# Optimization experiments

Hardware: AMD Instinct MI355X
Metric: run time of the kernel (lower is better)

## Reference

```python
import jax, jax.numpy as jnp
import numpy as np

M = 8192            # number of graphs (m)
NODES_PER_GRAPH = 64
N = M * NODES_PER_GRAPH  # total nodes (n)
D_H = 128
D_X = 128


def setup_inputs() -> dict:
    key = jax.random.key(0)
    k1, k2, k3 = jax.random.split(key, 3)
    # scale by 0.1 so the unstabilized exp(e) in segment_softmax stays finite in fp32
    h = 0.1 * jax.random.normal(k1, (M, D_H), dtype=jnp.float32)
    x = 0.1 * jax.random.normal(k2, (N, D_X), dtype=jnp.float32)
    a = jax.random.uniform(k3, (D_H, D_X), dtype=jnp.float32)  # th.rand init
    batch_num_nodes = jnp.full((M,), NODES_PER_GRAPH, dtype=jnp.int32)
    return {"h": h, "x": x, "a": a, "batch_num_nodes": batch_num_nodes}


def reference(h, x, a, batch_num_nodes):
    m = batch_num_nodes.shape[0]
    n = x.shape[0]
    # node -> graph segment ids (repeat_interleave of arange)
    seg = jnp.repeat(jnp.arange(m), batch_num_nodes, total_repeat_length=n)  # (n,)
    ha = (h @ a)[seg]                       # (n, d_x): gather per-graph query to nodes
    e = jnp.sum(x * ha, axis=1)             # (n,) attention logits
    ex = jnp.exp(e)                         # unstabilized exp, faithful to source
    z = jax.ops.segment_sum(ex, seg, num_segments=m)   # (m,) partition functions
    att = ex / z[seg]                       # (n,) segment softmax
    out = jax.ops.segment_sum(att[:, None] * x, seg, num_segments=m)  # (m, d_x)
    return out
```

## Files before the change

kernel.cpp:

```cpp
#include <hip/hip_runtime.h>


#define NPG  64
#define DDIM 128
#define SROW 132

typedef __attribute__((ext_vector_type(4))) float f32x4;

__global__ __launch_bounds__(256) void ha_gemm_kernel(
    const float* __restrict__ h, const float* __restrict__ a, float* __restrict__ ha)
{
    const int j    = threadIdx.x & 127;
    const int rg   = threadIdx.x >> 7;
    const int row0 = blockIdx.x * 8 + rg * 4;
    const float* hp = h + (size_t)row0 * DDIM;

    float acc0 = 0.f, acc1 = 0.f, acc2 = 0.f, acc3 = 0.f;
    #pragma unroll 8
    for (int k4 = 0; k4 < 32; ++k4) {
        f32x4 h0 = *(const f32x4*)(hp + 0 * DDIM + k4 * 4);
        f32x4 h1 = *(const f32x4*)(hp + 1 * DDIM + k4 * 4);
        f32x4 h2 = *(const f32x4*)(hp + 2 * DDIM + k4 * 4);
        f32x4 h3 = *(const f32x4*)(hp + 3 * DDIM + k4 * 4);
        #pragma unroll
        for (int kk = 0; kk < 4; ++kk) {
            float av = a[(k4 * 4 + kk) * DDIM + j];
            acc0 += h0[kk] * av;
            acc1 += h1[kk] * av;
            acc2 += h2[kk] * av;
            acc3 += h3[kk] * av;
        }
    }
    float* op = ha + (size_t)row0 * DDIM + j;
    op[0 * DDIM] = acc0; op[1 * DDIM] = acc1; op[2 * DDIM] = acc2; op[3 * DDIM] = acc3;
}

__global__ __launch_bounds__(256) void attn_kernel(
    const float* __restrict__ x, const float* __restrict__ ha, float* __restrict__ out)
{
    const int g = blockIdx.x;
    const int t = threadIdx.x;

    __shared__ __align__(16) float xs[NPG * SROW];
    __shared__ float exbuf[NPG];
    __shared__ float zbuf[4];
    __shared__ __align__(16) float opart[8][DDIM];

    const int qt = t & 3;
    const int i  = t >> 2;
    f32x4 qv[8];
    const float* qp = ha + (size_t)g * DDIM + qt * 32;
    #pragma unroll
    for (int c = 0; c < 8; ++c) qv[c] = *(const f32x4*)(qp + c * 4);

    const f32x4* xg = (const f32x4*)(x + (size_t)g * (NPG * DDIM));
    #pragma unroll
    for (int it = 0; it < 8; ++it) {
        int c = it * 256 + t;
        f32x4 v = xg[c];
        int row = c >> 5, col = c & 31;
        *(f32x4*)(&xs[row * SROW + col * 4]) = v;
    }
    __syncthreads();

    const float* xrow = &xs[i * SROW + qt * 32];
    float acc = 0.f;
    #pragma unroll
    for (int c = 0; c < 8; ++c) {
        f32x4 v = *(const f32x4*)(xrow + c * 4);
        acc += v[0] * qv[c][0] + v[1] * qv[c][1] + v[2] * qv[c][2] + v[3] * qv[c][3];
    }
    acc += __shfl_xor(acc, 1, 64);
    acc += __shfl_xor(acc, 2, 64);
    float ex = __expf(acc);
    float zw = ex;
    zw += __shfl_xor(zw, 4, 64);
    zw += __shfl_xor(zw, 8, 64);
    zw += __shfl_xor(zw, 16, 64);
    zw += __shfl_xor(zw, 32, 64);
    if (qt == 0)       exbuf[i] = ex;
    if ((t & 63) == 0) zbuf[t >> 6] = zw;
    __syncthreads();

    const float rz = 1.0f / (zbuf[0] + zbuf[1] + zbuf[2] + zbuf[3]);

    {
        const int jb  = (t & 31) * 4;
        const int grp = t >> 5;
        f32x4 o = {0.f, 0.f, 0.f, 0.f};
        #pragma unroll
        for (int k = 0; k < 8; ++k) {
            int node = grp * 8 + k;
            float w = exbuf[node] * rz;
            f32x4 v = *(const f32x4*)(&xs[node * SROW + jb]);
            o[0] += w * v[0]; o[1] += w * v[1]; o[2] += w * v[2]; o[3] += w * v[3];
        }
        *(f32x4*)(&opart[grp][jb]) = o;
    }
    __syncthreads();

    if (t < DDIM) {
        float o = 0.f;
        #pragma unroll
        for (int gq = 0; gq < 8; ++gq) o += opart[gq][t];
        out[(size_t)g * DDIM + t] = o;
    }
}

extern "C" void kernel_launch(void* const* d_in, const int* in_sizes, int n_in,
                              void* d_out, int out_size, void* d_ws, size_t ws_size,
                              hipStream_t stream) {
    const float* h = (const float*)d_in[0];
    const float* x = (const float*)d_in[1];
    const float* a = (const float*)d_in[2];
    float* out = (float*)d_out;
    float* ha  = (float*)d_ws;

    const int m = in_sizes[0] / DDIM;
    ha_gemm_kernel<<<m / 8, 256, 0, stream>>>(h, a, ha);
    attn_kernel<<<m, 256, 0, stream>>>(x, ha, out);
}
```

Before: 386.3 us.

## Keep node rows in registers and reduce weighted sum with wave shuffles

The attention kernel no longer stages the whole 64x128 graph tile in shared memory. Each thread loads its node's x slice directly into registers, computes the logit, and scales the slice by its softmax weight. The weighted sum is partially reduced across nodes with xor shuffles before a smaller shared-memory pass of 16 partials, and the launch bounds now request 6 blocks per CU. This cuts LDS traffic and footprint to raise occupancy, at the cost of many more shuffle instructions and higher register pressure.

```diff
diff --git a/kernel.cpp b/kernel.cpp
--- a/kernel.cpp
+++ b/kernel.cpp
@@ -3,7 +3,7 @@
 
 #define NPG  64
 #define DDIM 128
-#define SROW 132
+#define OROW 132
 
 typedef __attribute__((ext_vector_type(4))) float f32x4;
 
@@ -35,74 +35,71 @@
     op[0 * DDIM] = acc0; op[1 * DDIM] = acc1; op[2 * DDIM] = acc2; op[3 * DDIM] = acc3;
 }
 
-__global__ __launch_bounds__(256) void attn_kernel(
+__global__ __launch_bounds__(256, 6) void attn_kernel(
     const float* __restrict__ x, const float* __restrict__ ha, float* __restrict__ out)
 {
-    const int g = blockIdx.x;
-    const int t = threadIdx.x;
+    const int g  = blockIdx.x;
+    const int t  = threadIdx.x;
+    const int w  = t >> 6;
+    const int l  = t & 63;
+    const int i  = t >> 2;
+    const int qt = t & 3;
 
-    __shared__ __align__(16) float xs[NPG * SROW];
-    __shared__ float exbuf[NPG];
     __shared__ float zbuf[4];
-    __shared__ __align__(16) float opart[8][DDIM];
+    __shared__ __align__(16) float opart[16][OROW];
 
-    const int qt = t & 3;
-    const int i  = t >> 2;
-    f32x4 qv[8];
-    const float* qp = ha + (size_t)g * DDIM + qt * 32;
+    const float* xrow = x  + ((size_t)g * NPG + i) * DDIM;
+    const float* qrow = ha + (size_t)g * DDIM;
+    f32x4 xv[8];
     #pragma unroll
-    for (int c = 0; c < 8; ++c) qv[c] = *(const f32x4*)(qp + c * 4);
+    for (int c = 0; c < 8; ++c)
+        xv[c] = *(const f32x4*)(xrow + (qt + 4 * c) * 4);
 
-    const f32x4* xg = (const f32x4*)(x + (size_t)g * (NPG * DDIM));
-    #pragma unroll
-    for (int it = 0; it < 8; ++it) {
-        int c = it * 256 + t;
-        f32x4 v = xg[c];
-        int row = c >> 5, col = c & 31;
-        *(f32x4*)(&xs[row * SROW + col * 4]) = v;
-    }
-    __syncthreads();
-
-    const float* xrow = &xs[i * SROW + qt * 32];
-    float acc = 0.f;
+    float e = 0.f;
     #pragma unroll
     for (int c = 0; c < 8; ++c) {
-        f32x4 v = *(const f32x4*)(xrow + c * 4);
-        acc += v[0] * qv[c][0] + v[1] * qv[c][1] + v[2] * qv[c][2] + v[3] * qv[c][3];
+        f32x4 qv = *(const f32x4*)(qrow + (qt + 4 * c) * 4);
+        e += xv[c][0] * qv[0] + xv[c][1] * qv[1] + xv[c][2] * qv[2] + xv[c][3] * qv[3];
     }
-    acc += __shfl_xor(acc, 1, 64);
-    acc += __shfl_xor(acc, 2, 64);
-    float ex = __expf(acc);
+    e += __shfl_xor(e, 1, 64);
+    e += __shfl_xor(e, 2, 64);
+    float ex = __expf(e);
+
     float zw = ex;
     zw += __shfl_xor(zw, 4, 64);
     zw += __shfl_xor(zw, 8, 64);
     zw += __shfl_xor(zw, 16, 64);
     zw += __shfl_xor(zw, 32, 64);
-    if (qt == 0)       exbuf[i] = ex;
-    if ((t & 63) == 0) zbuf[t >> 6] = zw;
+    if (l == 0) zbuf[w] = zw;
     __syncthreads();
 
-    const float rz = 1.0f / (zbuf[0] + zbuf[1] + zbuf[2] + zbuf[3]);
+    const float rz  = 1.0f / (zbuf[0] + zbuf[1] + zbuf[2] + zbuf[3]);
+    const float att = ex * rz;
 
-    {
-        const int jb  = (t & 31) * 4;
-        const int grp = t >> 5;
-        f32x4 o = {0.f, 0.f, 0.f, 0.f};
+    #pragma unroll
+    for (int c = 0; c < 8; ++c) {
+        xv[c][0] *= att; xv[c][1] *= att; xv[c][2] *= att; xv[c][3] *= att;
+    }
+    #pragma unroll
+    for (int c = 0; c < 8; ++c) {
         #pragma unroll
-        for (int k = 0; k < 8; ++k) {
-            int node = grp * 8 + k;
-            float w = exbuf[node] * rz;
-            f32x4 v = *(const f32x4*)(&xs[node * SROW + jb]);
-            o[0] += w * v[0]; o[1] += w * v[1]; o[2] += w * v[2]; o[3] += w * v[3];
+        for (int u = 0; u < 4; ++u) {
+            xv[c][u] += __shfl_xor(xv[c][u], 4, 64);
+            xv[c][u] += __shfl_xor(xv[c][u], 8, 64);
         }
-        *(f32x4*)(&opart[grp][jb]) = o;
+    }
+    if (((l >> 2) & 3) == 0) {
+        const int blk = w * 4 + (l >> 4);
+        #pragma unroll
+        for (int c = 0; c < 8; ++c)
+            *(f32x4*)(&opart[blk][(qt + 4 * c) * 4]) = xv[c];
     }
     __syncthreads();
 
     if (t < DDIM) {
         float o = 0.f;
         #pragma unroll
-        for (int gq = 0; gq < 8; ++gq) o += opart[gq][t];
+        for (int p = 0; p < 16; ++p) o += opart[p][t];
         out[(size_t)g * DDIM + t] = o;
     }
 }
```

Result: no change. 386.6 us (+0.1%).
